# Kernel optimization log

Measured on AMD Instinct MI355X. Metric: run time of the kernel, lower is better.

## Reference

```python
import jax, jax.numpy as jnp
import numpy as np

K = 16            # neighbors
RATIO = 0.25      # sampling ratio -> M = N*RATIO
EPS = 1e-5        # BatchNorm eps


def _fps(pts, m):
    # Farthest point sampling for one cloud. pts: (N,3) -> (m,) int32 indices.
    n = pts.shape[0]

    def body(carry, _):
        dist, last = carry                      # dist: (N,) min sq-dist to selected set
        d = jnp.sum((pts - pts[last]) ** 2, axis=-1)
        dist = jnp.minimum(dist, d)
        nxt = jnp.argmax(dist).astype(jnp.int32)
        return (dist, nxt), nxt

    init = (jnp.full((n,), jnp.inf, pts.dtype), jnp.int32(0))
    _, rest = jax.lax.scan(body, init, None, length=m - 1)
    return jnp.concatenate([jnp.zeros((1,), jnp.int32), rest])


def setup_inputs() -> dict:
    key = jax.random.key(0)
    ks = jax.random.split(key, 3)
    B, N, C_IN, C_OUT = 8, 8192, 64, 128
    x = jax.random.normal(ks[0], (B, N, C_IN), jnp.float32)
    p = jax.random.normal(ks[1], (B, N, 3), jnp.float32)
    W = jax.random.normal(ks[2], (C_OUT, C_IN), jnp.float32) * 0.05
    gamma = jnp.ones((C_OUT,), jnp.float32)
    beta = jnp.zeros((C_OUT,), jnp.float32)
    run_mean = jnp.zeros((C_OUT,), jnp.float32)
    run_var = jnp.ones((C_OUT,), jnp.float32)
    return {"x": x, "p": p, "W": W, "gamma": gamma, "beta": beta,
            "run_mean": run_mean, "run_var": run_var}


def reference(x, p, W, gamma, beta, run_mean, run_var):
    B, N, _ = x.shape
    M = int(N * RATIO)

    # 1) FPS sample M points per cloud
    idx_fps = jax.vmap(lambda q: _fps(q, M))(p)                   # (B, M)
    p_out = jnp.take_along_axis(p, idx_fps[..., None], axis=1)    # (B, M, 3)

    # 2) KNN: squared distances (B, M, N), sorted K nearest via top_k on -dist
    d2 = (jnp.sum(p_out ** 2, -1)[..., None]
          + jnp.sum(p ** 2, -1)[:, None, :]
          - 2.0 * jnp.einsum('bmd,bnd->bmn', p_out, p))
    _, nbr = jax.lax.top_k(-d2, K)                                # (B, M, K) ascending dist

    # 3) Pointwise MLP: Conv1d(k=1, no bias) == matmul, then BN (eval) + ReLU
    h = jnp.einsum('bnc,oc->bno', x, W)                           # (B, N, C_OUT)
    h = (h - run_mean) * jax.lax.rsqrt(run_var + EPS) * gamma + beta
    h = jax.nn.relu(h)

    # 4) Gather neighbor features and max-pool over K
    flat = nbr.reshape(B, M * K)
    feats = jnp.take_along_axis(h, flat[..., None], axis=1).reshape(B, M, K, -1)
    y = jnp.max(feats, axis=2)                                    # (B, M, C_OUT)
    return y, p_out
```

## Files before the change

### kernel.cpp

```cpp
#include <hip/hip_runtime.h>

#define B_   8
#define N_   8192
#define CIN  64
#define COUT 128
#define M_   2048
#define K_   16

typedef float v2f __attribute__((ext_vector_type(2)));

template <int CTRL>
__device__ __forceinline__ unsigned long long dpp64(unsigned long long x) {
  int lo = (int)(unsigned)(x & 0xFFFFFFFFull);
  int hi = (int)(unsigned)(x >> 32);
  int dlo = __builtin_amdgcn_update_dpp(lo, lo, CTRL, 0xF, 0xF, false);
  int dhi = __builtin_amdgcn_update_dpp(hi, hi, CTRL, 0xF, 0xF, false);
  return ((unsigned long long)(unsigned)dhi << 32) | (unsigned)dlo;
}

__device__ __forceinline__ unsigned long long readlane_u64(unsigned long long k, int l) {
  unsigned lo = (unsigned)__builtin_amdgcn_readlane((int)(unsigned)(k & 0xFFFFFFFFull), l);
  unsigned hi = (unsigned)__builtin_amdgcn_readlane((int)(unsigned)(k >> 32), l);
  return ((unsigned long long)hi << 32) | lo;
}

__device__ __forceinline__ unsigned long long wave_min_u64(unsigned long long k) {
  unsigned long long t;
  t = dpp64<0x111>(k); k = t < k ? t : k;
  t = dpp64<0x112>(k); k = t < k ? t : k;
  t = dpp64<0x114>(k); k = t < k ? t : k;
  t = dpp64<0x118>(k); k = t < k ? t : k;
  t = dpp64<0x142>(k); k = t < k ? t : k;
  t = dpp64<0x143>(k); k = t < k ? t : k;
  return readlane_u64(k, 63);
}

#define FTH 256
#define FPT 32
#define MROWS2 16

__global__ __launch_bounds__(256) void fps_mlp_kernel(
    const float* __restrict__ p, float* __restrict__ p_out,
    const float* __restrict__ x, const float* __restrict__ W,
    const float* __restrict__ gamma, const float* __restrict__ beta,
    const float* __restrict__ rmean, const float* __restrict__ rvar,
    float* __restrict__ h) {
#pragma clang fp contract(off)
  __shared__ __align__(16) unsigned char smem[139776];

  const int tid = threadIdx.x;

  if (blockIdx.x >= 8) {
    float* wt = (float*)smem;
    float* xs = (float*)(smem + 33792);

    const int o  = tid & 127;
    const int rg = tid >> 7;
    const int rowBase = (blockIdx.x - 8) * MROWS2;

    for (int idx = tid; idx < COUT * CIN; idx += 256) {
      const int oo = idx >> 6, cc = idx & 63;
      wt[cc * 132 + oo] = W[idx];
    }
    ((float4*)xs)[tid] = ((const float4*)(x + (size_t)rowBase * CIN))[tid];
    __syncthreads();

    float acc[8] = {0.f, 0.f, 0.f, 0.f, 0.f, 0.f, 0.f, 0.f};
#pragma unroll
    for (int c4 = 0; c4 < CIN / 4; c4++) {
      const float w0 = wt[(4 * c4 + 0) * 132 + o];
      const float w1 = wt[(4 * c4 + 1) * 132 + o];
      const float w2 = wt[(4 * c4 + 2) * 132 + o];
      const float w3 = wt[(4 * c4 + 3) * 132 + o];
#pragma unroll
      for (int i = 0; i < 8; i++) {
        const float4 xv = *(const float4*)&xs[(rg * 8 + i) * CIN + c4 * 4];
        acc[i] += xv.x * w0 + xv.y * w1 + xv.z * w2 + xv.w * w3;
      }
    }
    const float mu = rmean[o];
    const float sc = rsqrtf(rvar[o] + 1e-5f) * gamma[o];
    const float bt = beta[o];
#pragma unroll
    for (int i = 0; i < 8; i++) {
      const float v = (acc[i] - mu) * sc + bt;
      h[(size_t)(rowBase + rg * 8 + i) * COUT + o] = fmaxf(v, 0.f);
    }
    return;
  }

  float4* pc4 = (float4*)smem;
  unsigned long long (*wred)[8] =
      (unsigned long long (*)[8])(smem + 131072);
  int* idxHist = (int*)(smem + 131072 + 128);

  const int b  = blockIdx.x;
  const int wv = tid >> 6;
  const int ln = tid & 63;

  const float* pb = p + (size_t)b * N_ * 3;
  for (int n = tid; n < N_; n += FTH)
    pc4[n] = make_float4(pb[3 * n + 0], pb[3 * n + 1], pb[3 * n + 2], 0.f);
  if (tid == 0) idxHist[0] = 0;
  __syncthreads();

  float4 c0 = pc4[0];
  float cx = c0.x, cy = c0.y, cz = c0.z;

  v2f X2[16], Y2[16], Z2[16], D2[16];
#pragma unroll
  for (int j = 0; j < 16; j++) {
    float4 a = pc4[tid + (2 * j) * FTH];
    float4 c = pc4[tid + (2 * j + 1) * FTH];
    X2[j] = (v2f){a.x, c.x};
    Y2[j] = (v2f){a.y, c.y};
    Z2[j] = (v2f){a.z, c.z};
    D2[j] = (v2f){__builtin_inff(), __builtin_inff()};
  }

  int buf = 0;
  for (int it = 1; it < M_; ++it) {
    const v2f cxv = {cx, cx}, cyv = {cy, cy}, czv = {cz, cz};
    v2f vbd = (v2f){-1.0f, -1.0f};
    int sx = 0, sy = 1;
#pragma unroll
    for (int j = 0; j < 16; j++) {
      v2f dx = X2[j] - cxv;
      v2f dy = Y2[j] - cyv;
      v2f dz = Z2[j] - czv;
      v2f m1 = dx * dx;
      v2f m2 = dy * dy;
      v2f s  = m1 + m2;
      v2f m3 = dz * dz;
      v2f d  = s + m3;
      v2f dm = __builtin_elementwise_min(D2[j], d);
      D2[j] = dm;
      const bool gx = dm.x > vbd.x;
      const bool gy = dm.y > vbd.y;
      sx = gx ? (2 * j) : sx;
      sy = gy ? (2 * j + 1) : sy;
      vbd = __builtin_elementwise_max(vbd, dm);
    }
    float bd; int bk;
    if (vbd.y > vbd.x || (vbd.y == vbd.x && sy < sx)) { bd = vbd.y; bk = sy; }
    else                                               { bd = vbd.x; bk = sx; }
    const int n = tid + (bk << 8);
    unsigned long long key =
        ((unsigned long long)__float_as_uint(bd) << 32) |
        (unsigned)(N_ - 1 - n);

    {
      unsigned long long t;
      t = dpp64<0x111>(key); key = t > key ? t : key;
      t = dpp64<0x112>(key); key = t > key ? t : key;
      t = dpp64<0x114>(key); key = t > key ? t : key;
      t = dpp64<0x118>(key); key = t > key ? t : key;
      t = dpp64<0x142>(key); key = t > key ? t : key;
      t = dpp64<0x143>(key); key = t > key ? t : key;
    }
    if (ln == 63) wred[buf][wv] = key;
    __syncthreads();
    unsigned long long kk = wred[buf][ln & 3];
    unsigned long long t;
    t = dpp64<0x111>(kk); kk = t > kk ? t : kk;
    t = dpp64<0x112>(kk); kk = t > kk ? t : kk;
    const int nw = N_ - 1 -
        (int)(unsigned)__builtin_amdgcn_readlane((int)(unsigned)(kk & 0xFFFFFFFFull), 3);
    float4 cc = pc4[nw];
    cx = cc.x; cy = cc.y; cz = cc.z;
    if (tid == 0) idxHist[it] = nw;
    buf ^= 1;
  }
  __syncthreads();

  float* po = p_out + (size_t)b * M_ * 3;
  for (int mi = tid; mi < M_; mi += FTH) {
    float4 v = pc4[idxHist[mi]];
    po[mi * 3 + 0] = v.x;
    po[mi * 3 + 1] = v.y;
    po[mi * 3 + 2] = v.z;
  }
}

#define UMAXK 0xFFFFFFFFFFFFFFFFull
#define QPB  16

__global__ __launch_bounds__(1024) void knn_kernel(
    const float* __restrict__ p, const float* __restrict__ p_out,
    const float* __restrict__ h, float* __restrict__ y) {
#pragma clang fp contract(off)
  __shared__ float4 pc4[N_];
  __shared__ int winLds[QPB][K_];

  const int t    = threadIdx.x;
  const int wv   = t >> 6;
  const int lane = t & 63;
  const int b    = blockIdx.x & 7;
  const int grp  = blockIdx.x >> 3;
  const int q    = b * M_ + grp * QPB + wv;

  const float* pb = p + (size_t)b * N_ * 3;
  for (int n = t; n < N_; n += 1024) {
    float xx = pb[3 * n + 0], yy = pb[3 * n + 1], zz = pb[3 * n + 2];
    float sn = (xx * xx + yy * yy) + zz * zz;
    pc4[n] = make_float4(xx, yy, zz, sn);
  }
  __syncthreads();

  const float qx = p_out[q * 3 + 0];
  const float qy = p_out[q * 3 + 1];
  const float qz = p_out[q * 3 + 2];
  const float sq = (qx * qx + qy * qy) + qz * qz;

  unsigned long long c0 = UMAXK, c1 = UMAXK, c2 = UMAXK, c3 = UMAXK;
#pragma unroll 4
  for (int j = 0; j < 128; j++) {
    const int n = lane + (j << 6);
    float4 v = pc4[n];
    float dot = __builtin_fmaf(qz, v.z,
                __builtin_fmaf(qy, v.y, qx * v.x));
    float d2 = (sq + v.w) - 2.0f * dot;
    unsigned u = __float_as_uint(d2);
    u ^= (unsigned)((int)u >> 31) | 0x80000000u;
    unsigned long long key = ((unsigned long long)u << 32) | (unsigned)n;
    if (key < c3) {
      unsigned long long x2 = key, mn;
      mn = x2 < c0 ? x2 : c0; x2 = x2 < c0 ? c0 : x2; c0 = mn;
      mn = x2 < c1 ? x2 : c1; x2 = x2 < c1 ? c1 : x2; c1 = mn;
      mn = x2 < c2 ? x2 : c2; x2 = x2 < c2 ? c2 : x2; c2 = mn;
      c3 = x2 < c3 ? x2 : c3;
    }
  }

  int count = 4;
  unsigned long long em0 = 0ull, em1 = 0ull;
  unsigned long long mykey = UMAXK;

  for (int k = 0; k < K_; k++) {
    unsigned long long cnd = (count > 0) ? c0 : UMAXK;
    unsigned long long win = wave_min_u64(cnd);
    if (lane == k) mykey = win;
    const int nstar = (int)(unsigned)(win & 0xFFFFFFFFu);
    if ((nstar & 63) == lane) {
      const int j = nstar >> 6;
      if (j < 64) em0 |= 1ull << j; else em1 |= 1ull << (j - 64);
      c0 = c1; c1 = c2; c2 = c3; c3 = UMAXK; count--;
      if (count == 0 && k < K_ - 1) {
        c0 = c1 = c2 = c3 = UMAXK;
        for (int j2 = 0; j2 < 128; j2++) {
          bool ex = (j2 < 64) ? ((em0 >> j2) & 1ull) : ((em1 >> (j2 - 64)) & 1ull);
          if (!ex) {
            const int n2 = lane + (j2 << 6);
            float4 v = pc4[n2];
            float dot = __builtin_fmaf(qz, v.z,
                        __builtin_fmaf(qy, v.y, qx * v.x));
            float d2 = (sq + v.w) - 2.0f * dot;
            unsigned u = __float_as_uint(d2);
            u ^= (unsigned)((int)u >> 31) | 0x80000000u;
            unsigned long long kk2 = ((unsigned long long)u << 32) | (unsigned)n2;
            if (kk2 < c3) {
              unsigned long long x2 = kk2, mn;
              mn = x2 < c0 ? x2 : c0; x2 = x2 < c0 ? c0 : x2; c0 = mn;
              mn = x2 < c1 ? x2 : c1; x2 = x2 < c1 ? c1 : x2; c1 = mn;
              mn = x2 < c2 ? x2 : c2; x2 = x2 < c2 ? c2 : x2; c2 = mn;
              c3 = x2 < c3 ? x2 : c3;
            }
          }
        }
        count = 4;
      }
    }
  }

  if (lane < K_) winLds[wv][lane] = (int)(unsigned)(mykey & 0xFFFFFFFFu);
  __syncthreads();

  const float* hb = h + (size_t)b * N_ * COUT;
  float2 acc = make_float2(-__builtin_inff(), -__builtin_inff());
#pragma unroll
  for (int i = 0; i < K_; i++) {
    const int n = winLds[wv][i];
    float2 v = *(const float2*)(hb + (size_t)n * COUT + lane * 2);
    acc.x = fmaxf(acc.x, v.x);
    acc.y = fmaxf(acc.y, v.y);
  }
  *(float2*)(y + (size_t)q * COUT + lane * 2) = acc;
}

extern "C" void kernel_launch(void* const* d_in, const int* in_sizes, int n_in,
                              void* d_out, int out_size, void* d_ws, size_t ws_size,
                              hipStream_t stream) {
  const float* x     = (const float*)d_in[0];
  const float* p     = (const float*)d_in[1];
  const float* W     = (const float*)d_in[2];
  const float* gamma = (const float*)d_in[3];
  const float* beta  = (const float*)d_in[4];
  const float* rmean = (const float*)d_in[5];
  const float* rvar  = (const float*)d_in[6];

  float* y     = (float*)d_out;
  float* p_out = y + (size_t)B_ * M_ * COUT;
  float* h     = (float*)d_ws;

  fps_mlp_kernel<<<8 + (B_ * N_) / MROWS2, 256, 0, stream>>>(
      p, p_out, x, W, gamma, beta, rmean, rvar, h);
  knn_kernel<<<B_ * (M_ / QPB), 1024, 0, stream>>>(p, p_out, h, y);
}
```

Measured before the change: 1.988 ms.

## Sort FPS points into Morton-ordered cells and skip distance updates via bounding-box pruning

Each cloud's points are bucketed into a 512-cell Morton grid with a histogram, a prefix scan and a scatter into shared memory. Each thread then owns four spatially coherent 8-point blocks with bounding boxes. Per FPS iteration, a block's distance update is skipped when the box's lower-bound distance to the new centroid exceeds the block's current max min-distance, so the cached key is reused. The argmax key packs distance, original index and sorted slot, and the final 4-wave reduction reads shared memory directly instead of using DPP. This adds setup cost and branch divergence, and relies on a 1.0001 slack factor for correct pruning.

```diff
diff --git a/kernel.cpp b/kernel.cpp
--- a/kernel.cpp
+++ b/kernel.cpp
@@ -8,24 +8,26 @@
 #define K_   16
 
 typedef float v2f __attribute__((ext_vector_type(2)));
+typedef unsigned int v2u __attribute__((ext_vector_type(2)));
+typedef unsigned long long ull;
 
 template <int CTRL>
-__device__ __forceinline__ unsigned long long dpp64(unsigned long long x) {
+__device__ __forceinline__ ull dpp64(ull x) {
   int lo = (int)(unsigned)(x & 0xFFFFFFFFull);
   int hi = (int)(unsigned)(x >> 32);
   int dlo = __builtin_amdgcn_update_dpp(lo, lo, CTRL, 0xF, 0xF, false);
   int dhi = __builtin_amdgcn_update_dpp(hi, hi, CTRL, 0xF, 0xF, false);
-  return ((unsigned long long)(unsigned)dhi << 32) | (unsigned)dlo;
-}
-
-__device__ __forceinline__ unsigned long long readlane_u64(unsigned long long k, int l) {
+  return ((ull)(unsigned)dhi << 32) | (unsigned)dlo;
+}
+
+__device__ __forceinline__ ull readlane_u64(ull k, int l) {
   unsigned lo = (unsigned)__builtin_amdgcn_readlane((int)(unsigned)(k & 0xFFFFFFFFull), l);
   unsigned hi = (unsigned)__builtin_amdgcn_readlane((int)(unsigned)(k >> 32), l);
-  return ((unsigned long long)hi << 32) | lo;
-}
-
-__device__ __forceinline__ unsigned long long wave_min_u64(unsigned long long k) {
-  unsigned long long t;
+  return ((ull)hi << 32) | lo;
+}
+
+__device__ __forceinline__ ull wave_min_u64(ull k) {
+  ull t;
   t = dpp64<0x111>(k); k = t < k ? t : k;
   t = dpp64<0x112>(k); k = t < k ? t : k;
   t = dpp64<0x114>(k); k = t < k ? t : k;
@@ -35,11 +37,22 @@
   return readlane_u64(k, 63);
 }
 
+__device__ __forceinline__ int cell9(float x, float y, float z) {
+  int qx = (int)fminf(fmaxf(floorf(x + 4.f), 0.f), 7.f);
+  int qy = (int)fminf(fmaxf(floorf(y + 4.f), 0.f), 7.f);
+  int qz = (int)fminf(fmaxf(floorf(z + 4.f), 0.f), 7.f);
+  int m = 0;
+#pragma unroll
+  for (int k = 0; k < 3; k++)
+    m |= (((qx >> k) & 1) << (3 * k + 2)) | (((qy >> k) & 1) << (3 * k + 1)) |
+         (((qz >> k) & 1) << (3 * k));
+  return m;
+}
+
 #define FTH 256
-#define FPT 32
 #define MROWS2 16
 
-__global__ __launch_bounds__(256) void fps_mlp_kernel(
+__global__ __launch_bounds__(256, 1) void fps_mlp_kernel(
     const float* __restrict__ p, float* __restrict__ p_out,
     const float* __restrict__ x, const float* __restrict__ W,
     const float* __restrict__ gamma, const float* __restrict__ beta,
@@ -89,68 +102,116 @@
     return;
   }
 
-  float4* pc4 = (float4*)smem;
-  unsigned long long (*wred)[8] =
-      (unsigned long long (*)[8])(smem + 131072);
-  int* idxHist = (int*)(smem + 131072 + 128);
+  float4* spc = (float4*)smem;
+  ull (*wred)[4] = (ull (*)[4])(smem + 131072);
+  int* hA  = (int*)(smem + 131200);
+  int* hB  = (int*)(smem + 133248);
+  int* cur = (int*)(smem + 135296);
 
   const int b  = blockIdx.x;
   const int wv = tid >> 6;
   const int ln = tid & 63;
-
   const float* pb = p + (size_t)b * N_ * 3;
-  for (int n = tid; n < N_; n += FTH)
-    pc4[n] = make_float4(pb[3 * n + 0], pb[3 * n + 1], pb[3 * n + 2], 0.f);
-  if (tid == 0) idxHist[0] = 0;
-  __syncthreads();
-
-  float4 c0 = pc4[0];
-  float cx = c0.x, cy = c0.y, cz = c0.z;
-
+
+  for (int i = tid; i < 512; i += 256) hA[i] = 0;
+  __syncthreads();
+  for (int n = tid; n < N_; n += 256) {
+    float xx = pb[3 * n], yy = pb[3 * n + 1], zz = pb[3 * n + 2];
+    atomicAdd(&hA[cell9(xx, yy, zz)], 1);
+  }
+  __syncthreads();
+  {
+    int* src = hA; int* dst = hB;
+    for (int off = 1; off < 512; off <<= 1) {
+      for (int i = tid; i < 512; i += 256)
+        dst[i] = src[i] + (i >= off ? src[i - off] : 0);
+      __syncthreads();
+      int* t = src; src = dst; dst = t;
+    }
+    for (int i = tid; i < 512; i += 256)
+      cur[i] = (i ? src[i - 1] : 0);
+  }
+  __syncthreads();
+  for (int n = tid; n < N_; n += 256) {
+    float xx = pb[3 * n], yy = pb[3 * n + 1], zz = pb[3 * n + 2];
+    int pos = atomicAdd(&cur[cell9(xx, yy, zz)], 1);
+    spc[pos] = make_float4(xx, yy, zz, __int_as_float(n));
+  }
+  __syncthreads();
+
+  float cx = pb[0], cy = pb[1], cz = pb[2];
+  float* po = p_out + (size_t)b * M_ * 3;
+  if (tid == 0) { po[0] = cx; po[1] = cy; po[2] = cz; }
+
+  const float INF = __builtin_inff();
   v2f X2[16], Y2[16], Z2[16], D2[16];
-#pragma unroll
-  for (int j = 0; j < 16; j++) {
-    float4 a = pc4[tid + (2 * j) * FTH];
-    float4 c = pc4[tid + (2 * j + 1) * FTH];
-    X2[j] = (v2f){a.x, c.x};
-    Y2[j] = (v2f){a.y, c.y};
-    Z2[j] = (v2f){a.z, c.z};
-    D2[j] = (v2f){__builtin_inff(), __builtin_inff()};
-  }
+  v2u LO2[16];
+  float blox[4], bhix[4], bloy[4], bhiy[4], bloz[4], bhiz[4];
+  ull skey[4]; float bdm[4];
+#pragma unroll
+  for (int s = 0; s < 4; s++) {
+    const int Bq = s * 256 + ln * 4 + wv;
+    float lx = INF, hx = -INF, ly = INF, hy = -INF,
+          lz = INF, hz = -INF;
+#pragma unroll
+    for (int e = 0; e < 8; e++) {
+      float4 P = spc[Bq * 8 + e];
+      const int jj = s * 4 + (e >> 1);
+      const unsigned no = (unsigned)__float_as_int(P.w);
+      const unsigned lo =
+          (((unsigned)(N_ - 1) - no) << 13) | (unsigned)(Bq * 8 + e);
+      if ((e & 1) == 0) { X2[jj].x = P.x; Y2[jj].x = P.y; Z2[jj].x = P.z; LO2[jj].x = lo; }
+      else              { X2[jj].y = P.x; Y2[jj].y = P.y; Z2[jj].y = P.z; LO2[jj].y = lo; }
+      lx = fminf(lx, P.x); hx = fmaxf(hx, P.x);
+      ly = fminf(ly, P.y); hy = fmaxf(hy, P.y);
+      lz = fminf(lz, P.z); hz = fmaxf(hz, P.z);
+    }
+    blox[s] = lx; bhix[s] = hx; bloy[s] = ly; bhiy[s] = hy;
+    bloz[s] = lz; bhiz[s] = hz;
+    skey[s] = 0ull; bdm[s] = INF;
+  }
+#pragma unroll
+  for (int j = 0; j < 16; j++) D2[j] = (v2f){INF, INF};
 
   int buf = 0;
   for (int it = 1; it < M_; ++it) {
     const v2f cxv = {cx, cx}, cyv = {cy, cy}, czv = {cz, cz};
-    v2f vbd = (v2f){-1.0f, -1.0f};
-    int sx = 0, sy = 1;
-#pragma unroll
-    for (int j = 0; j < 16; j++) {
-      v2f dx = X2[j] - cxv;
-      v2f dy = Y2[j] - cyv;
-      v2f dz = Z2[j] - czv;
-      v2f m1 = dx * dx;
-      v2f m2 = dy * dy;
-      v2f s  = m1 + m2;
-      v2f m3 = dz * dz;
-      v2f d  = s + m3;
-      v2f dm = __builtin_elementwise_min(D2[j], d);
-      D2[j] = dm;
-      const bool gx = dm.x > vbd.x;
-      const bool gy = dm.y > vbd.y;
-      sx = gx ? (2 * j) : sx;
-      sy = gy ? (2 * j + 1) : sy;
-      vbd = __builtin_elementwise_max(vbd, dm);
-    }
-    float bd; int bk;
-    if (vbd.y > vbd.x || (vbd.y == vbd.x && sy < sx)) { bd = vbd.y; bk = sy; }
-    else                                               { bd = vbd.x; bk = sx; }
-    const int n = tid + (bk << 8);
-    unsigned long long key =
-        ((unsigned long long)__float_as_uint(bd) << 32) |
-        (unsigned)(N_ - 1 - n);
+#pragma unroll
+    for (int s = 0; s < 4; s++) {
+      const float ux = fmaxf(fmaxf(blox[s] - cx, cx - bhix[s]), 0.f);
+      const float uy = fmaxf(fmaxf(bloy[s] - cy, cy - bhiy[s]), 0.f);
+      const float uz = fmaxf(fmaxf(bloz[s] - cz, cz - bhiz[s]), 0.f);
+      const float lb2 = (ux * ux + uy * uy) + uz * uz;
+      if (lb2 <= bdm[s]) {
+        ull rk = 0ull;
+#pragma unroll
+        for (int q = 0; q < 4; q++) {
+          const int jj = s * 4 + q;
+          v2f dx = X2[jj] - cxv;
+          v2f dy = Y2[jj] - cyv;
+          v2f dz = Z2[jj] - czv;
+          v2f m1 = dx * dx;
+          v2f m2 = dy * dy;
+          v2f ss = m1 + m2;
+          v2f m3 = dz * dz;
+          v2f d  = ss + m3;
+          v2f dm = __builtin_elementwise_min(D2[jj], d);
+          D2[jj] = dm;
+          ull ka = ((ull)__float_as_uint(dm.x) << 32) | (ull)LO2[jj].x;
+          rk = ka > rk ? ka : rk;
+          ull kb = ((ull)__float_as_uint(dm.y) << 32) | (ull)LO2[jj].y;
+          rk = kb > rk ? kb : rk;
+        }
+        skey[s] = rk;
+        bdm[s] = __uint_as_float((unsigned)(rk >> 32)) * 1.0001f;
+      }
+    }
+    ull k0 = skey[0] > skey[1] ? skey[0] : skey[1];
+    ull k1 = skey[2] > skey[3] ? skey[2] : skey[3];
+    ull key = k0 > k1 ? k0 : k1;
 
     {
-      unsigned long long t;
+      ull t;
       t = dpp64<0x111>(key); key = t > key ? t : key;
       t = dpp64<0x112>(key); key = t > key ? t : key;
       t = dpp64<0x114>(key); key = t > key ? t : key;
@@ -160,25 +221,16 @@
     }
     if (ln == 63) wred[buf][wv] = key;
     __syncthreads();
-    unsigned long long kk = wred[buf][ln & 3];
-    unsigned long long t;
-    t = dpp64<0x111>(kk); kk = t > kk ? t : kk;
-    t = dpp64<0x112>(kk); kk = t > kk ? t : kk;
-    const int nw = N_ - 1 -
-        (int)(unsigned)__builtin_amdgcn_readlane((int)(unsigned)(kk & 0xFFFFFFFFull), 3);
-    float4 cc = pc4[nw];
+    const ulonglong2* wp = (const ulonglong2*)&wred[buf][0];
+    ulonglong2 A = wp[0], Bb = wp[1];
+    ull w0 = A.x > A.y ? A.x : A.y;
+    ull w1 = Bb.x > Bb.y ? Bb.x : Bb.y;
+    ull ww = w0 > w1 ? w0 : w1;
+    const int ns = (int)(ww & 0x1FFFull);
+    float4 cc = spc[ns];
     cx = cc.x; cy = cc.y; cz = cc.z;
-    if (tid == 0) idxHist[it] = nw;
+    if (tid == 0) { po[3 * it] = cx; po[3 * it + 1] = cy; po[3 * it + 2] = cz; }
     buf ^= 1;
-  }
-  __syncthreads();
-
-  float* po = p_out + (size_t)b * M_ * 3;
-  for (int mi = tid; mi < M_; mi += FTH) {
-    float4 v = pc4[idxHist[mi]];
-    po[mi * 3 + 0] = v.x;
-    po[mi * 3 + 1] = v.y;
-    po[mi * 3 + 2] = v.z;
   }
 }
 
```

Result: slower. 2.235 ms (+12.4%).
